# Performance work log

Hardware: AMD Instinct MI355X
Metric: run time of the kernel (lower is better)

## Reference

```python
import jax, jax.numpy as jnp
import numpy as np

B, S, D, L = 32, 1024, 768, 12

def setup_inputs() -> dict:
    key = jax.random.key(0)
    ks = jax.random.split(key, 10)
    hidden_states = jax.random.normal(ks[0], (B, S, D), dtype=jnp.float32)
    Wq = jax.random.normal(ks[1], (L, D, D), dtype=jnp.float32) * 0.02
    Wk = jax.random.normal(ks[2], (L, D, D), dtype=jnp.float32) * 0.02
    Wv = jax.random.normal(ks[3], (L, D, D), dtype=jnp.float32) * 0.02
    bq = jnp.zeros((L, D), dtype=jnp.float32)
    bk = jnp.zeros((L, D), dtype=jnp.float32)
    bv = jnp.zeros((L, D), dtype=jnp.float32)
    l_k = jnp.full((L, D), 0.8, dtype=jnp.float32)  # iA3 scales, init 0.8 per source
    l_v = jnp.full((L, D), 0.8, dtype=jnp.float32)
    W_head = jax.random.normal(ks[4], (D, 1), dtype=jnp.float32) * 0.02
    b_head = jnp.zeros((1,), dtype=jnp.float32)
    return {"hidden_states": hidden_states, "Wq": Wq, "bq": bq, "Wk": Wk, "bk": bk,
            "Wv": Wv, "bv": bv, "l_k": l_k, "l_v": l_v, "W_head": W_head, "b_head": b_head}

def reference(hidden_states, Wq, bq, Wk, bk, Wv, bv, l_k, l_v, W_head, b_head):
    scale = 1.0 / jnp.sqrt(jnp.float32(D))

    def layer_step(h, params):
        wq, bq_i, wk, bk_i, wv, bv_i, lk, lv = params
        Q = jnp.einsum('bsd,de->bse', h, wq) + bq_i
        K = (jnp.einsum('bsd,de->bse', h, wk) + bk_i) * lk  # iA3 per-channel scale on K
        V = (jnp.einsum('bsd,de->bse', h, wv) + bv_i) * lv  # iA3 per-channel scale on V
        attn = jax.nn.softmax(jnp.einsum('bqd,bkd->bqk', Q, K) * scale, axis=-1)
        h_new = jnp.einsum('bqk,bkd->bqd', attn, V)  # note: no residual/LN, matches source
        return h_new, None

    h, _ = jax.lax.scan(layer_step, hidden_states, (Wq, bq, Wk, bk, Wv, bv, l_k, l_v))
    pooled = h[:, 0, :]  # CLS token
    out = pooled @ W_head + b_head  # [B, 1]
    return out[:, 0]
```

## Files before the change

### kernel.cpp

```cpp
#include <hip/hip_runtime.h>
#include <hip/hip_fp16.h>
#include <math.h>

#define B_ 32
#define S_ 1024
#define D_ 768
#define L_ 12
#define SD 786432LL
#define SS 1048576LL
#define DD 589824LL
#define LDL 1769472LL

typedef _Float16 half8 __attribute__((ext_vector_type(8)));
typedef float f32x4 __attribute__((ext_vector_type(4)));
typedef unsigned short u16;

#define SW(lr) ((((lr) ^ ((lr) >> 3)) & 7))

#define GLD16(p, o) __builtin_amdgcn_global_load_lds( \
        (const __attribute__((address_space(1))) void*)(p), \
        (__attribute__((address_space(3))) void*)&smem[o], 16, 0, 0)

__global__ __launch_bounds__(256, 2)
void gemm_qkv_k(const __half* __restrict__ A, const __half* __restrict__ Wt,
                const float* __restrict__ biasC, const float* __restrict__ scaleC,
                float aBias,
                __half* __restrict__ CQ, __half* __restrict__ CK, __half* __restrict__ CVt,
                int nBase, int tilesX, int mPerXcd)
{
    __shared__ __align__(16) u16 smem[16384];
    const int K = 768;

    const int flat = blockIdx.x;
    const int xcd = flat & 7;
    const int jj = flat >> 3;
    const int mLocal = jj / tilesX;
    const int nxI = jj - mLocal * tilesX;
    const int n0 = nxI * 128;
    const int m0 = (xcd * mPerXcd + mLocal) * 128;

    const int t = threadIdx.x;
    const int l = t & 63, w = t >> 6;
    const int wm = (w & 1) * 64, wn = (w >> 1) * 64;

    const int u0 = t, u1 = t + 256;
    const int r0 = u0 >> 2, c0 = (u0 & 3) ^ ((r0 >> 1) & 3);
    const int r1 = u1 >> 2, c1 = (u1 & 3) ^ ((r1 >> 1) & 3);
    const __half* gA0 = A + (long long)(m0 + r0) * K + c0 * 8;
    const __half* gA1 = A + (long long)(m0 + r1) * K + c1 * 8;
    const __half* gB0 = Wt + (long long)(n0 + r0) * K + c0 * 8;
    const __half* gB1 = Wt + (long long)(n0 + r1) * K + c1 * 8;

    int aoff[4], boff[4];
    const int kc = l >> 4;
    #pragma unroll
    for (int mt = 0; mt < 4; ++mt) {
        int rr = wm + mt * 16 + (l & 15);
        aoff[mt] = (rr * 4 + (kc ^ ((rr >> 1) & 3))) * 8;
        int rb = wn + mt * 16 + (l & 15);
        boff[mt] = (rb * 4 + (kc ^ ((rb >> 1) & 3))) * 8;
    }

    f32x4 acc[4][4];
    #pragma unroll
    for (int i = 0; i < 4; ++i)
        #pragma unroll
        for (int j = 0; j < 4; ++j)
            acc[i][j] = (f32x4){0.f, 0.f, 0.f, 0.f};

    GLD16(gA0, u0 * 8);         GLD16(gA1, u1 * 8);
    GLD16(gB0, 8192 + u0 * 8);  GLD16(gB1, 8192 + u1 * 8);
    asm volatile("s_waitcnt vmcnt(0)\n\ts_barrier" ::: "memory");

    int cur = 0;
    for (int k0 = 0; k0 < K; k0 += 32) {
        const int sa = cur * 4096, sb = 8192 + cur * 4096;
        half8 af[4], bf[4];
        #pragma unroll
        for (int mt = 0; mt < 4; ++mt) af[mt] = *(const half8*)(const void*)&smem[sa + aoff[mt]];
        #pragma unroll
        for (int nt = 0; nt < 4; ++nt) bf[nt] = *(const half8*)(const void*)&smem[sb + boff[nt]];
        __builtin_amdgcn_sched_barrier(0);
        if (k0 + 32 < K) {
            const int nsa = (cur ^ 1) * 4096, nsb = 8192 + (cur ^ 1) * 4096;
            GLD16(gA0 + k0 + 32, nsa + u0 * 8);  GLD16(gA1 + k0 + 32, nsa + u1 * 8);
            GLD16(gB0 + k0 + 32, nsb + u0 * 8);  GLD16(gB1 + k0 + 32, nsb + u1 * 8);
        }
        #pragma unroll
        for (int nt = 0; nt < 4; ++nt)
            #pragma unroll
            for (int mt = 0; mt < 4; ++mt)
                acc[mt][nt] = __builtin_amdgcn_mfma_f32_16x16x32_f16(af[mt], bf[nt], acc[mt][nt], 0, 0, 0);
        asm volatile("s_waitcnt vmcnt(0)\n\ts_barrier" ::: "memory");
        cur ^= 1;
    }

    const int nCat0 = n0 + nBase;
    const int region = nCat0 / 768;
    const int colBase = nCat0 - region * 768;

    float badd[4], bmul[4];
    #pragma unroll
    for (int nt = 0; nt < 4; ++nt) {
        int gn = nCat0 + wn + nt * 16 + (l & 15);
        badd[nt] = aBias * biasC[gn];
        bmul[nt] = scaleC[gn];
    }

    const int qbase = w * 4096;
    #pragma unroll
    for (int mt = 0; mt < 4; ++mt) {
        #pragma unroll
        for (int nt = 0; nt < 4; ++nt) {
            #pragma unroll
            for (int i = 0; i < 4; ++i) {
                int lrow = mt * 16 + ((l >> 4) << 2) + i;
                int lcol = nt * 16 + (l & 15);
                float v = (acc[mt][nt][i] + badd[nt]) * bmul[nt];
                int cc = lcol >> 3, c7 = lcol & 7;
                smem[qbase + lrow * 64 + ((cc ^ SW(lrow)) << 3) + c7] =
                    __half_as_ushort(__float2half(v));
            }
        }
    }
    __syncthreads();

    if (region < 2) {
        __half* Creg = region ? CK : CQ;
        #pragma unroll
        for (int p = 0; p < 8; ++p) {
            int u = t + p * 256;
            int R = u >> 4, cc = u & 15;
            int qb = ((R >> 6) + ((cc >> 3) << 1)) * 4096;
            int lr = R & 63, lcc = cc & 7;
            half8 val = *(const half8*)(const void*)&smem[qb + lr * 64 + ((lcc ^ SW(lr)) << 3)];
            *(half8*)(void*)&Creg[(long long)(m0 + R) * 768 + colBase + cc * 8] = val;
        }
    } else {
        #pragma unroll
        for (int p = 0; p < 8; ++p) {
            int u = t + p * 256;
            int Crow = u >> 4, mcc = u & 15;
            __align__(16) u16 tmp[8];
            #pragma unroll
            for (int j = 0; j < 8; ++j) {
                int m = mcc * 8 + j;
                int qb = ((m >> 6) + ((Crow >> 6) << 1)) * 4096;
                int lr = m & 63, lcol = Crow & 63;
                int lcc = lcol >> 3;
                tmp[j] = smem[qb + lr * 64 + ((lcc ^ SW(lr)) << 3) + (lcol & 7)];
            }
            long long b = m0 >> 10;
            __half* dst = CVt + b * SD + (long long)(colBase + Crow) * 1024 + (m0 & 1023) + mcc * 8;
            *(half8*)(void*)dst = *(const half8*)(const void*)tmp;
        }
    }
}

template<int SWIZ, int MODE>
__global__ __launch_bounds__(256, 2)
void gemm_att_k(const __half* __restrict__ A, const __half* __restrict__ B,
                float aAcc, __half* __restrict__ C, int K, int ldc,
                long long sA, long long sB, long long sC,
                int tilesX, int tilesPB, int bpx,
                float* __restrict__ rsp, const float* __restrict__ invsum)
{
    __shared__ __align__(16) u16 smem[16384];
    __shared__ float sums[128 * 17];

    int nxI, ny;
    long long bz;
    if (SWIZ) {
        int flat = blockIdx.x;
        int xcd = flat & 7;
        int j = flat >> 3;
        int bLocal = j / tilesPB;
        int tt = j - bLocal * tilesPB;
        bz = (long long)(xcd * bpx + bLocal);
        ny = tt / tilesX;
        nxI = tt - ny * tilesX;
    } else {
        nxI = blockIdx.x; ny = blockIdx.y; bz = blockIdx.z;
    }

    const int t = threadIdx.x;
    const int l = t & 63, w = t >> 6;
    const int n0 = nxI * 128;
    const int m0 = ny * 128;
    A += bz * sA; B += bz * sB; C += bz * sC;

    const int wm = (w & 1) * 64, wn = (w >> 1) * 64;

    const int u0 = t, u1 = t + 256;
    const int r0 = u0 >> 2, c0 = (u0 & 3) ^ ((r0 >> 1) & 3);
    const int r1 = u1 >> 2, c1 = (u1 & 3) ^ ((r1 >> 1) & 3);
    const __half* gA0 = A + (long long)(m0 + r0) * K + c0 * 8;
    const __half* gA1 = A + (long long)(m0 + r1) * K + c1 * 8;
    const __half* gB0 = B + (long long)(n0 + r0) * K + c0 * 8;
    const __half* gB1 = B + (long long)(n0 + r1) * K + c1 * 8;

    int aoff[4], boff[4];
    const int kc = l >> 4;
    #pragma unroll
    for (int mt = 0; mt < 4; ++mt) {
        int rr = wm + mt * 16 + (l & 15);
        aoff[mt] = (rr * 4 + (kc ^ ((rr >> 1) & 3))) * 8;
        int rb = wn + mt * 16 + (l & 15);
        boff[mt] = (rb * 4 + (kc ^ ((rb >> 1) & 3))) * 8;
    }

    f32x4 acc[4][4];
    #pragma unroll
    for (int i = 0; i < 4; ++i)
        #pragma unroll
        for (int j = 0; j < 4; ++j)
            acc[i][j] = (f32x4){0.f, 0.f, 0.f, 0.f};

    GLD16(gA0, u0 * 8);         GLD16(gA1, u1 * 8);
    GLD16(gB0, 8192 + u0 * 8);  GLD16(gB1, 8192 + u1 * 8);
    asm volatile("s_waitcnt vmcnt(0)\n\ts_barrier" ::: "memory");

    int cur = 0;
    for (int k0 = 0; k0 < K; k0 += 32) {
        const int sa = cur * 4096, sb = 8192 + cur * 4096;
        half8 af[4], bf[4];
        #pragma unroll
        for (int mt = 0; mt < 4; ++mt) af[mt] = *(const half8*)(const void*)&smem[sa + aoff[mt]];
        #pragma unroll
        for (int nt = 0; nt < 4; ++nt) bf[nt] = *(const half8*)(const void*)&smem[sb + boff[nt]];
        __builtin_amdgcn_sched_barrier(0);
        if (k0 + 32 < K) {
            const int nsa = (cur ^ 1) * 4096, nsb = 8192 + (cur ^ 1) * 4096;
            GLD16(gA0 + k0 + 32, nsa + u0 * 8);  GLD16(gA1 + k0 + 32, nsa + u1 * 8);
            GLD16(gB0 + k0 + 32, nsb + u0 * 8);  GLD16(gB1 + k0 + 32, nsb + u1 * 8);
        }
        #pragma unroll
        for (int nt = 0; nt < 4; ++nt)
            #pragma unroll
            for (int mt = 0; mt < 4; ++mt)
                acc[mt][nt] = __builtin_amdgcn_mfma_f32_16x16x32_f16(af[mt], bf[nt], acc[mt][nt], 0, 0, 0);
        asm volatile("s_waitcnt vmcnt(0)\n\ts_barrier" ::: "memory");
        cur ^= 1;
    }

    float invr[4][4];
    if (MODE == 2) {
        #pragma unroll
        for (int mt = 0; mt < 4; ++mt)
            #pragma unroll
            for (int i = 0; i < 4; ++i)
                invr[mt][i] = invsum[bz * 1024 + m0 + wm + mt * 16 + ((l >> 4) << 2) + i];
    }

    const int qbase = w * 4096;
    #pragma unroll
    for (int mt = 0; mt < 4; ++mt) {
        #pragma unroll
        for (int nt = 0; nt < 4; ++nt) {
            #pragma unroll
            for (int i = 0; i < 4; ++i) {
                int lrow = mt * 16 + ((l >> 4) << 2) + i;
                int lcol = nt * 16 + (l & 15);
                float v;
                if (MODE == 1)      v = __expf(acc[mt][nt][i] * aAcc);
                else                v = acc[mt][nt][i] * aAcc * invr[mt][i];
                int cc = lcol >> 3, c7 = lcol & 7;
                smem[qbase + lrow * 64 + ((cc ^ SW(lrow)) << 3) + c7] =
                    __half_as_ushort(__float2half(v));
            }
        }
    }
    __syncthreads();

    #pragma unroll
    for (int p = 0; p < 8; ++p) {
        int u = t + p * 256;
        int R = u >> 4, cc = u & 15;
        int qb = ((R >> 6) + ((cc >> 3) << 1)) * 4096;
        int lr = R & 63, lcc = cc & 7;
        half8 val = *(const half8*)(const void*)&smem[qb + lr * 64 + ((lcc ^ SW(lr)) << 3)];
        *(half8*)(void*)&C[(long long)(m0 + R) * ldc + n0 + cc * 8] = val;
        if (MODE == 1) {
            float s8 = 0.f;
            #pragma unroll
            for (int j = 0; j < 8; ++j) s8 += (float)val[j];
            sums[R * 17 + cc] = s8;
        }
    }
    if (MODE == 1) {
        __syncthreads();
        if (t < 128) {
            float s = 0.f;
            #pragma unroll
            for (int c = 0; c < 16; ++c) s += sums[t * 17 + c];
            rsp[bz * 8192 + (long long)(m0 + t) * 8 + nxI] = s;
        }
    }
}

__global__ __launch_bounds__(256)
void rowsuminv_k(const float* __restrict__ rsp, float* __restrict__ inv, int n)
{
    int i = blockIdx.x * 256 + threadIdx.x;
    if (i < n) {
        const float* p = rsp + (long long)i * 8;
        float s = ((p[0] + p[1]) + (p[2] + p[3])) + ((p[4] + p[5]) + (p[6] + p[7]));
        inv[i] = 1.0f / s;
    }
}

__global__ __launch_bounds__(256)
void cvt32to16_k(const float* __restrict__ X, __half* __restrict__ Y)
{
    long long i = ((long long)blockIdx.x * 256 + threadIdx.x) * 4;
    float4 v = *(const float4*)&X[i];
    *(__half2*)&Y[i]     = __floats2half2_rn(v.x, v.y);
    *(__half2*)&Y[i + 2] = __floats2half2_rn(v.z, v.w);
}

__global__ __launch_bounds__(256)
void wtrans_k(const float* __restrict__ W, __half* __restrict__ Wt,
              long long ldL, int rowOff)
{
    __shared__ float Ls[64][65];
    const int lyr = blockIdx.z;
    const int k0 = blockIdx.y * 64, n0 = blockIdx.x * 64;
    const float* src = W + (long long)lyr * DD;
    __half* dst = Wt + (long long)lyr * ldL;
    const int t = threadIdx.x;
    #pragma unroll
    for (int p = 0; p < 4; ++p) {
        int u = t + p * 256;
        int r = u >> 4, c4 = (u & 15) * 4;
        float4 v = *(const float4*)&src[(long long)(k0 + r) * D_ + n0 + c4];
        Ls[r][c4] = v.x; Ls[r][c4 + 1] = v.y; Ls[r][c4 + 2] = v.z; Ls[r][c4 + 3] = v.w;
    }
    __syncthreads();
    #pragma unroll
    for (int p = 0; p < 2; ++p) {
        int u = t + p * 256;
        int n = u >> 3, kc8 = (u & 7) * 8;
        __align__(16) u16 tmp[8];
        #pragma unroll
        for (int j = 0; j < 8; ++j) {
            _Float16 h = (_Float16)Ls[kc8 + j][n];
            tmp[j] = *(const u16*)&h;
        }
        *(half8*)(void*)&dst[(long long)(rowOff + n0 + n) * D_ + k0 + kc8] =
            *(const half8*)(const void*)tmp;
    }
}

__global__ __launch_bounds__(256)
void bscat_k(const float* __restrict__ bq, const float* __restrict__ bk,
             const float* __restrict__ bv, const float* __restrict__ lk,
             const float* __restrict__ lv, float* __restrict__ bsb,
             float* __restrict__ bss)
{
    int i = blockIdx.x * 256 + threadIdx.x;
    if (i >= L_ * 2304) return;
    int l = i / 2304, p = i - l * 2304;
    int r = p / 768, c = p - r * 768;
    float b, s;
    if (r == 0)      { b = bq[l * 768 + c]; s = 1.f; }
    else if (r == 1) { b = bk[l * 768 + c]; s = lk[l * 768 + c]; }
    else             { b = bv[l * 768 + c]; s = lv[l * 768 + c]; }
    bsb[i] = b; bss[i] = s;
}

__global__ __launch_bounds__(256)
void q0_k(const __half* __restrict__ H16, const __half* __restrict__ Wcat,
          const float* __restrict__ bq, float* __restrict__ q0f, float sig)
{
    const int b = blockIdx.x;
    const int n = blockIdx.y * 256 + threadIdx.x;
    const int t = threadIdx.x;
    __shared__ __half hrow[768];
    const __half* h = H16 + (long long)b * SD;
    hrow[t] = h[t]; hrow[t + 256] = h[t + 256]; hrow[t + 512] = h[t + 512];
    __syncthreads();
    const __half* wr = Wcat + 11LL * LDL + (long long)n * 768;
    float acc = 0.f;
    for (int k = 0; k < 768; ++k) acc += (float)hrow[k] * (float)wr[k];
    q0f[b * 768 + n] = acc + sig * bq[11 * 768 + n];
}

__global__ __launch_bounds__(256)
void s0_k(const float* __restrict__ q0f, const __half* __restrict__ K16,
          float* __restrict__ s0f, int b0, float aQK)
{
    const int z = blockIdx.x;
    const int b = b0 + z;
    const int s = blockIdx.y * 256 + threadIdx.x;
    const int t = threadIdx.x;
    __shared__ float qrow[768];
    qrow[t] = q0f[b * 768 + t];
    qrow[t + 256] = q0f[b * 768 + t + 256];
    qrow[t + 512] = q0f[b * 768 + t + 512];
    __syncthreads();
    const __half* kr = K16 + (long long)z * SD + (long long)s * 768;
    float acc = 0.f;
    for (int k = 0; k < 768; ++k) acc += qrow[k] * (float)kr[k];
    s0f[b * 1024 + s] = acc * aQK;
}

__global__ __launch_bounds__(256)
void sm0_k(float* __restrict__ s0f, int b0)
{
    float* p = s0f + (long long)(b0 + blockIdx.x) * 1024;
    const int t = threadIdx.x;
    float v[4];
    float mx = -1e30f;
    #pragma unroll
    for (int j = 0; j < 4; ++j) { v[j] = p[t + 256 * j]; mx = fmaxf(mx, v[j]); }
    __shared__ float red[256];
    red[t] = mx; __syncthreads();
    for (int s = 128; s > 0; s >>= 1) { if (t < s) red[t] = fmaxf(red[t], red[t + s]); __syncthreads(); }
    mx = red[0];
    __syncthreads();
    float sum = 0.f;
    #pragma unroll
    for (int j = 0; j < 4; ++j) { v[j] = __expf(v[j] - mx); sum += v[j]; }
    red[t] = sum; __syncthreads();
    for (int s = 128; s > 0; s >>= 1) { if (t < s) red[t] += red[t + s]; __syncthreads(); }
    const float inv = 1.0f / red[0];
    __syncthreads();
    #pragma unroll
    for (int j = 0; j < 4; ++j) p[t + 256 * j] = v[j] * inv;
}

__global__ __launch_bounds__(256)
void o0_k(const float* __restrict__ p0f, const __half* __restrict__ Vt16,
          float* __restrict__ o0f, int b0, float invSig)
{
    const int z = blockIdx.x;
    const int b = b0 + z;
    const int d = blockIdx.y * 256 + threadIdx.x;
    const int t = threadIdx.x;
    __shared__ float prow[1024];
    #pragma unroll
    for (int j = 0; j < 4; ++j) prow[t + 256 * j] = p0f[b * 1024 + t + 256 * j];
    __syncthreads();
    const __half* vr = Vt16 + (long long)z * SD + (long long)d * 1024;
    float acc = 0.f;
    for (int s = 0; s < 1024; ++s) acc += prow[s] * (float)vr[s];
    o0f[b * 768 + d] = acc * invSig;
}

__global__ __launch_bounds__(256)
void headf_k(const float* __restrict__ o0f, const float* __restrict__ Wh,
             const float* __restrict__ bh, float* __restrict__ out)
{
    const int b = blockIdx.x;
    const int t = threadIdx.x;
    float s = 0.f;
    for (int d = t; d < 768; d += 256) s += o0f[b * 768 + d] * Wh[d];
    __shared__ float red[256];
    red[t] = s; __syncthreads();
    for (int k = 128; k > 0; k >>= 1) { if (t < k) red[t] += red[t + k]; __syncthreads(); }
    if (t == 0) out[b] = red[0] + bh[0];
}

extern "C" void kernel_launch(void* const* d_in, const int* in_sizes, int n_in,
                              void* d_out, int out_size, void* d_ws, size_t ws_size,
                              hipStream_t stream)
{
    const float* hs = (const float*)d_in[0];
    const float* Wq = (const float*)d_in[1];
    const float* bq = (const float*)d_in[2];
    const float* Wk = (const float*)d_in[3];
    const float* bk = (const float*)d_in[4];
    const float* Wv = (const float*)d_in[5];
    const float* bv = (const float*)d_in[6];
    const float* lk = (const float*)d_in[7];
    const float* lv = (const float*)d_in[8];
    const float* Wh = (const float*)d_in[9];
    const float* bh = (const float*)d_in[10];
    float* outp = (float*)d_out;

    __half* H16  = (__half*)d_ws;
    __half* Wcat = H16 + (long long)B_ * SD;
    float*  bsb  = (float*)(Wcat + 12LL * LDL);
    float*  bss  = bsb + 12 * 2304;
    float*  q0f  = bss + 12 * 2304;
    float*  s0f  = q0f + 32 * 768;
    float*  o0f  = s0f + 32 * 1024;
    float*  rsp  = o0f + 32 * 768;
    float*  inv  = rsp + 32LL * 8192;
    __half* Q16  = (__half*)(inv + 32 * 1024);

    const size_t baseBytes = (size_t)((char*)Q16 - (char*)d_ws);
    const size_t perG = ((size_t)(3 * SD) + (size_t)SS) * 2;
    long long avail = (long long)ws_size - (long long)baseBytes;
    int G = (avail > 0) ? (int)(avail / perG) : 1;
    if (G >= 32) G = 32; else if (G >= 16) G = 16; else if (G >= 8) G = 8;
    if (G < 1) G = 1;
    __half* K16  = Q16 + (long long)G * SD;
    __half* Vt16 = K16 + (long long)G * SD;
    __half* P16  = Vt16 + (long long)G * SD;

    cvt32to16_k<<<dim3((int)((B_ * SD) / 1024)), 256, 0, stream>>>(hs, H16);
    wtrans_k<<<dim3(12, 12, 12), 256, 0, stream>>>(Wq, Wcat, LDL, 0);
    wtrans_k<<<dim3(12, 12, 12), 256, 0, stream>>>(Wk, Wcat, LDL, 768);
    wtrans_k<<<dim3(12, 12, 12), 256, 0, stream>>>(Wv, Wcat, LDL, 1536);
    bscat_k<<<dim3((L_ * 2304 + 255) / 256), 256, 0, stream>>>(bq, bk, bv, lk, lv, bsb, bss);

    const float scq = 0.036084391824351615f;
    float sig = 1.f;

    for (int lyr = 0; lyr < L_ - 1; ++lyr) {
        const __half* W = Wcat + (long long)lyr * LDL;
        const float* bb = bsb + lyr * 2304;
        const float* ss = bss + lyr * 2304;
        const float aQK = scq / (sig * sig);

        for (int b0 = 0; b0 < B_; b0 += G) {
            const int nb = (B_ - b0 < G) ? (B_ - b0) : G;
            const __half* hg = H16 + (long long)b0 * SD;

            gemm_qkv_k<<<dim3(18 * 8 * nb), 256, 0, stream>>>(
                hg, W, bb, ss, sig, Q16, K16, Vt16, 0, 18, nb);

            if ((nb & 7) == 0) {
                gemm_att_k<1, 1><<<dim3(nb * 64), 256, 0, stream>>>(
                    Q16, K16, aQK, P16, 768, 1024, SD, SD, SS, 8, 64, nb >> 3, rsp, nullptr);
            } else {
                gemm_att_k<0, 1><<<dim3(8, 8, nb), 256, 0, stream>>>(
                    Q16, K16, aQK, P16, 768, 1024, SD, SD, SS, 8, 64, 1, rsp, nullptr);
            }

            rowsuminv_k<<<dim3(nb * 4), 256, 0, stream>>>(rsp, inv, nb * 1024);

            if ((nb & 7) == 0) {
                gemm_att_k<1, 2><<<dim3(nb * 48), 256, 0, stream>>>(
                    P16, Vt16, 4.f, H16 + (long long)b0 * SD, 1024, 768, SS, SD, SD,
                    6, 48, nb >> 3, nullptr, inv);
            } else {
                gemm_att_k<0, 2><<<dim3(6, 8, nb), 256, 0, stream>>>(
                    P16, Vt16, 4.f, H16 + (long long)b0 * SD, 1024, 768, SS, SD, SD,
                    6, 48, 1, nullptr, inv);
            }
        }
        sig *= 4.f;
    }

    const float aQK = scq / (sig * sig);
    q0_k<<<dim3(B_, 3), 256, 0, stream>>>(H16, Wcat, bq, q0f, sig);

    for (int b0 = 0; b0 < B_; b0 += G) {
        const int nb = (B_ - b0 < G) ? (B_ - b0) : G;
        const __half* hg = H16 + (long long)b0 * SD;

        gemm_qkv_k<<<dim3(12 * 8 * nb), 256, 0, stream>>>(
            hg, Wcat + 11LL * LDL + 768LL * 768, bsb + 11 * 2304, bss + 11 * 2304,
            sig, K16 , K16, Vt16, 768, 12, nb);

        s0_k<<<dim3(nb, 4), 256, 0, stream>>>(q0f, K16, s0f, b0, aQK);
        sm0_k<<<dim3(nb), 256, 0, stream>>>(s0f, b0);
        o0_k<<<dim3(nb, 3), 256, 0, stream>>>(s0f, Vt16, o0f, b0, 1.f / sig);
    }

    headf_k<<<dim3(B_), 256, 0, stream>>>(o0f, Wh, bh, outp);
}
```

Measured before the change: 3.623 ms.

## Triple-buffer LDS in GEMM kernels with one barrier per k-step

Both GEMM kernels move from double to triple buffering of the A/B tiles in LDS. Loads are now issued two k-steps ahead and each iteration waits with vmcnt(4) instead of draining all outstanding loads, leaving one barrier per iteration instead of two. LDS grows to 48KB per block, and the softmax sums scratch is aliased into the enlarged buffer. Launch bounds are raised to 3 blocks per CU, which tightens the register budget and may force spills.

```diff
diff --git a/kernel.cpp b/kernel.cpp
--- a/kernel.cpp
+++ b/kernel.cpp
@@ -21,14 +21,15 @@
         (const __attribute__((address_space(1))) void*)(p), \
         (__attribute__((address_space(3))) void*)&smem[o], 16, 0, 0)
 
-__global__ __launch_bounds__(256, 2)
+
+__global__ __launch_bounds__(256, 3)
 void gemm_qkv_k(const __half* __restrict__ A, const __half* __restrict__ Wt,
                 const float* __restrict__ biasC, const float* __restrict__ scaleC,
                 float aBias,
                 __half* __restrict__ CQ, __half* __restrict__ CK, __half* __restrict__ CVt,
                 int nBase, int tilesX, int mPerXcd)
 {
-    __shared__ __align__(16) u16 smem[16384];
+    __shared__ __align__(16) u16 smem[24576];
     const int K = 768;
 
     const int flat = blockIdx.x;
@@ -68,32 +69,37 @@
         for (int j = 0; j < 4; ++j)
             acc[i][j] = (f32x4){0.f, 0.f, 0.f, 0.f};
 
-    GLD16(gA0, u0 * 8);         GLD16(gA1, u1 * 8);
-    GLD16(gB0, 8192 + u0 * 8);  GLD16(gB1, 8192 + u1 * 8);
-    asm volatile("s_waitcnt vmcnt(0)\n\ts_barrier" ::: "memory");
+    GLD16(gA0,      u0 * 8);                 GLD16(gA1,      u1 * 8);
+    GLD16(gB0,      12288 + u0 * 8);         GLD16(gB1,      12288 + u1 * 8);
+    GLD16(gA0 + 32, 4096 + u0 * 8);          GLD16(gA1 + 32, 4096 + u1 * 8);
+    GLD16(gB0 + 32, 12288 + 4096 + u0 * 8);  GLD16(gB1 + 32, 12288 + 4096 + u1 * 8);
 
     int cur = 0;
+    #pragma unroll 3
     for (int k0 = 0; k0 < K; k0 += 32) {
-        const int sa = cur * 4096, sb = 8192 + cur * 4096;
+        if (k0 + 32 < K) asm volatile("s_waitcnt vmcnt(4)\n\ts_barrier" ::: "memory");
+        else             asm volatile("s_waitcnt vmcnt(0)\n\ts_barrier" ::: "memory");
+        if (k0 + 64 < K) {
+            const int ts = (cur + 2 >= 3) ? (cur - 1) : (cur + 2);
+            const int tsa = ts * 4096, tsb = 12288 + ts * 4096;
+            GLD16(gA0 + k0 + 64, tsa + u0 * 8);  GLD16(gA1 + k0 + 64, tsa + u1 * 8);
+            GLD16(gB0 + k0 + 64, tsb + u0 * 8);  GLD16(gB1 + k0 + 64, tsb + u1 * 8);
+        }
+        const int sa = cur * 4096, sb = 12288 + cur * 4096;
         half8 af[4], bf[4];
         #pragma unroll
         for (int mt = 0; mt < 4; ++mt) af[mt] = *(const half8*)(const void*)&smem[sa + aoff[mt]];
         #pragma unroll
         for (int nt = 0; nt < 4; ++nt) bf[nt] = *(const half8*)(const void*)&smem[sb + boff[nt]];
-        __builtin_amdgcn_sched_barrier(0);
-        if (k0 + 32 < K) {
-            const int nsa = (cur ^ 1) * 4096, nsb = 8192 + (cur ^ 1) * 4096;
-            GLD16(gA0 + k0 + 32, nsa + u0 * 8);  GLD16(gA1 + k0 + 32, nsa + u1 * 8);
-            GLD16(gB0 + k0 + 32, nsb + u0 * 8);  GLD16(gB1 + k0 + 32, nsb + u1 * 8);
-        }
         #pragma unroll
         for (int nt = 0; nt < 4; ++nt)
             #pragma unroll
             for (int mt = 0; mt < 4; ++mt)
                 acc[mt][nt] = __builtin_amdgcn_mfma_f32_16x16x32_f16(af[mt], bf[nt], acc[mt][nt], 0, 0, 0);
-        asm volatile("s_waitcnt vmcnt(0)\n\ts_barrier" ::: "memory");
-        cur ^= 1;
-    }
+        __builtin_amdgcn_sched_barrier(0);
+        cur = (cur >= 2) ? 0 : (cur + 1);
+    }
+    __syncthreads();
 
     const int nCat0 = n0 + nBase;
     const int region = nCat0 / 768;
@@ -158,15 +164,15 @@
 }
 
 template<int SWIZ, int MODE>
-__global__ __launch_bounds__(256, 2)
+__global__ __launch_bounds__(256, 3)
 void gemm_att_k(const __half* __restrict__ A, const __half* __restrict__ B,
                 float aAcc, __half* __restrict__ C, int K, int ldc,
                 long long sA, long long sB, long long sC,
                 int tilesX, int tilesPB, int bpx,
                 float* __restrict__ rsp, const float* __restrict__ invsum)
 {
-    __shared__ __align__(16) u16 smem[16384];
-    __shared__ float sums[128 * 17];
+    __shared__ __align__(16) u16 smem[24576];
+    float* sums = (float*)(void*)&smem[16384];
 
     int nxI, ny;
     long long bz;
@@ -216,32 +222,37 @@
         for (int j = 0; j < 4; ++j)
             acc[i][j] = (f32x4){0.f, 0.f, 0.f, 0.f};
 
-    GLD16(gA0, u0 * 8);         GLD16(gA1, u1 * 8);
-    GLD16(gB0, 8192 + u0 * 8);  GLD16(gB1, 8192 + u1 * 8);
-    asm volatile("s_waitcnt vmcnt(0)\n\ts_barrier" ::: "memory");
+    GLD16(gA0,      u0 * 8);                 GLD16(gA1,      u1 * 8);
+    GLD16(gB0,      12288 + u0 * 8);         GLD16(gB1,      12288 + u1 * 8);
+    GLD16(gA0 + 32, 4096 + u0 * 8);          GLD16(gA1 + 32, 4096 + u1 * 8);
+    GLD16(gB0 + 32, 12288 + 4096 + u0 * 8);  GLD16(gB1 + 32, 12288 + 4096 + u1 * 8);
 
     int cur = 0;
+    #pragma unroll 3
     for (int k0 = 0; k0 < K; k0 += 32) {
-        const int sa = cur * 4096, sb = 8192 + cur * 4096;
+        if (k0 + 32 < K) asm volatile("s_waitcnt vmcnt(4)\n\ts_barrier" ::: "memory");
+        else             asm volatile("s_waitcnt vmcnt(0)\n\ts_barrier" ::: "memory");
+        if (k0 + 64 < K) {
+            const int ts = (cur + 2 >= 3) ? (cur - 1) : (cur + 2);
+            const int tsa = ts * 4096, tsb = 12288 + ts * 4096;
+            GLD16(gA0 + k0 + 64, tsa + u0 * 8);  GLD16(gA1 + k0 + 64, tsa + u1 * 8);
+            GLD16(gB0 + k0 + 64, tsb + u0 * 8);  GLD16(gB1 + k0 + 64, tsb + u1 * 8);
+        }
+        const int sa = cur * 4096, sb = 12288 + cur * 4096;
         half8 af[4], bf[4];
         #pragma unroll
         for (int mt = 0; mt < 4; ++mt) af[mt] = *(const half8*)(const void*)&smem[sa + aoff[mt]];
         #pragma unroll
         for (int nt = 0; nt < 4; ++nt) bf[nt] = *(const half8*)(const void*)&smem[sb + boff[nt]];
-        __builtin_amdgcn_sched_barrier(0);
-        if (k0 + 32 < K) {
-            const int nsa = (cur ^ 1) * 4096, nsb = 8192 + (cur ^ 1) * 4096;
-            GLD16(gA0 + k0 + 32, nsa + u0 * 8);  GLD16(gA1 + k0 + 32, nsa + u1 * 8);
-            GLD16(gB0 + k0 + 32, nsb + u0 * 8);  GLD16(gB1 + k0 + 32, nsb + u1 * 8);
-        }
         #pragma unroll
         for (int nt = 0; nt < 4; ++nt)
             #pragma unroll
             for (int mt = 0; mt < 4; ++mt)
                 acc[mt][nt] = __builtin_amdgcn_mfma_f32_16x16x32_f16(af[mt], bf[nt], acc[mt][nt], 0, 0, 0);
-        asm volatile("s_waitcnt vmcnt(0)\n\ts_barrier" ::: "memory");
-        cur ^= 1;
-    }
+        __builtin_amdgcn_sched_barrier(0);
+        cur = (cur >= 2) ? 0 : (cur + 1);
+    }
+    __syncthreads();
 
     float invr[4][4];
     if (MODE == 2) {
```

Result: faster. 3.482 ms (-3.9%).
